# Optimization experiments

Hardware: AMD Instinct MI355X
Metric: run time of the kernel (lower is better)

## Reference

```python
import jax, jax.numpy as jnp
import numpy as np

B, G, K, KD = 16384, 17, 12, 16      # batch, games, kicks/game, kick feature dim
DK, DM, H, T = 16, 32, 2, 4          # d_kick, d_model, n_attn_heads, n_targets
SD, H1, H2, HH = 64, 256, 128, 32    # static_dim, backbone hidden dims, head hidden
AO = H * DM                          # attention output dim = 64
EPS = 1e-5
NEG_INF = float('-inf')


def setup_inputs() -> dict:
    ks = jax.random.split(jax.random.key(0), 18)
    n = lambda i, s, sc=0.05: jax.random.normal(ks[i], s, jnp.float32) * sc
    x_static = jax.random.normal(ks[0], (B, SD), jnp.float32)
    x_kicks = jax.random.normal(ks[1], (B, G, K, KD), jnp.float32)
    # masks: True = real game / kick; force position 0 valid so no row is fully padded
    outer_mask = jax.random.bernoulli(ks[2], 0.9, (B, G)).at[:, 0].set(True)
    inner_mask = jax.random.bernoulli(ks[3], 0.85, (B, G, K)).at[:, :, 0].set(True)
    return dict(
        x_static=x_static, x_kicks=x_kicks,
        W_ke=n(4, (KD, DK)), b_ke=jnp.zeros((DK,), jnp.float32),
        q_inner=n(5, (1, DK), 0.02),
        W_ge=n(6, (DK, DM)), b_ge=jnp.zeros((DM,), jnp.float32),
        pos_emb=n(7, (G, DM), 0.02),
        q_outer=n(8, (T * H, DM), 0.02),
        log_temp=jnp.zeros((T,), jnp.float32),
        ln_g=jnp.ones((T, AO), jnp.float32), ln_b=jnp.zeros((T, AO), jnp.float32),
        W1=n(9, (SD, H1)), b1=jnp.zeros((H1,), jnp.float32),
        g1=jnp.ones((H1,), jnp.float32), be1=jnp.zeros((H1,), jnp.float32),
        m1=n(10, (H1,)), v1=jax.random.uniform(ks[11], (H1,), jnp.float32) + 0.5,
        W2=n(12, (H1, H2)), b2=jnp.zeros((H2,), jnp.float32),
        g2=jnp.ones((H2,), jnp.float32), be2=jnp.zeros((H2,), jnp.float32),
        m2=n(13, (H2,)), v2=jax.random.uniform(ks[14], (H2,), jnp.float32) + 0.5,
        Wh1=n(15, (T, H2 + AO, HH)), bh1=jnp.zeros((T, HH), jnp.float32),
        Wh2=n(16, (T, HH)), bh2=jnp.zeros((T,), jnp.float32),
        outer_mask=outer_mask, inner_mask=inner_mask)


def _forward(x_static, x_kicks, W_ke, b_ke, q_inner, W_ge, b_ge, pos_emb,
             q_outer, log_temp, ln_g, ln_b, W1, b1, g1, be1, m1, v1,
             W2, b2, g2, be2, m2, v2, Wh1, bh1, Wh2, bh2,
             outer_mask, inner_mask):
    # kick encoder: Linear -> ReLU, [B,G,K,KD] -> [B,G,K,DK]
    kick_enc = jax.nn.relu(jnp.einsum('bgkd,de->bgke', x_kicks, W_ke) + b_ke)
    # inner AttentionPool: single learned query over kicks within each game
    ai = jnp.einsum('d,bgkd->bgk', q_inner[0], kick_enc) * (DK ** -0.5)
    ai = jnp.where(inner_mask, ai, NEG_INF)
    wi = jnp.nan_to_num(jax.nn.softmax(ai, axis=-1))       # all-masked rows -> 0
    per_game = jnp.einsum('bgk,bgkd->bgd', wi, kick_enc)   # [B,G,DK]
    # game encoder + learned positional embedding
    encoded = jax.nn.relu(per_game @ W_ge + b_ge) + pos_emb[None]  # [B,G,DM]
    # outer AttentionPool: T*H learned queries over games, per-target temperature
    ao = jnp.einsum('qd,bgd->bqg', q_outer, encoded) * (DM ** -0.5)
    ao = ao * jnp.repeat(jnp.exp(-log_temp), H)[None, :, None]
    ao = jnp.where(outer_mask[:, None, :], ao, NEG_INF)
    wo = jnp.nan_to_num(jax.nn.softmax(ao, axis=-1))
    pooled = jnp.einsum('bqg,bgd->bqd', wo, encoded).reshape(-1, T, AO)  # [B,T,64]
    # per-target LayerNorm on history vector
    mu = pooled.mean(-1, keepdims=True)
    var = ((pooled - mu) ** 2).mean(-1, keepdims=True)
    hist = (pooled - mu) * jax.lax.rsqrt(var + EPS) * ln_g[None] + ln_b[None]
    # backbone: Linear -> BatchNorm(eval) -> ReLU, x2 (dropout = identity in eval)
    z = jax.nn.relu((x_static @ W1 + b1 - m1) * jax.lax.rsqrt(v1 + EPS) * g1 + be1)
    z = jax.nn.relu((z @ W2 + b2 - m2) * jax.lax.rsqrt(v2 + EPS) * g2 + be2)
    # per-target heads on [shared_static ; history_vec]
    head_in = jnp.concatenate(
        [jnp.broadcast_to(z[:, None, :], (z.shape[0], T, H2)), hist], axis=-1)  # [B,T,192]
    h = jax.nn.relu(jnp.einsum('btd,tdh->bth', head_in, Wh1) + bh1[None])
    out = jnp.einsum('bth,th->bt', h, Wh2) + bh2[None]
    return jnp.maximum(out, 0.0)  # all targets non-negative (clamp, not softplus)


def reference(x_static, x_kicks, W_ke, b_ke, q_inner, W_ge, b_ge, pos_emb,
              q_outer, log_temp, ln_g, ln_b, W1, b1, g1, be1, m1, v1,
              W2, b2, g2, be2, m2, v2, Wh1, bh1, Wh2, bh2,
              outer_mask, inner_mask):
    return _forward(x_static, x_kicks, W_ke, b_ke, q_inner, W_ge, b_ge, pos_emb,
                    q_outer, log_temp, ln_g, ln_b, W1, b1, g1, be1, m1, v1,
                    W2, b2, g2, be2, m2, v2, Wh1, bh1, Wh2, bh2,
                    outer_mask, inner_mask)
```

## Files before the change

### kernel.cpp

```cpp
#include <hip/hip_runtime.h>
#include <math.h>

#define NEGM (-1e30f)

typedef __fp16 f16x4 __attribute__((ext_vector_type(4)));
typedef __fp16 f16x2 __attribute__((ext_vector_type(2)));
typedef float  f32x4 __attribute__((ext_vector_type(4)));

__device__ __forceinline__ float4 ld4(const float* p) { return *(const float4*)p; }
__device__ __forceinline__ void fma4(float4& a, float s, const float4 w) {
    a.x += s * w.x; a.y += s * w.y; a.z += s * w.z; a.w += s * w.w;
}

__global__ __launch_bounds__(64) void hist_kernel(
    const float* __restrict__ x_kicks,
    const float* __restrict__ W_ke, const float* __restrict__ b_ke,
    const float* __restrict__ q_inner,
    const float* __restrict__ W_ge, const float* __restrict__ b_ge,
    const float* __restrict__ pos_emb, const float* __restrict__ q_outer,
    const float* __restrict__ log_temp,
    const float* __restrict__ ln_g, const float* __restrict__ ln_b,
    const int* __restrict__ outer_mask, const int* __restrict__ inner_mask,
    float* __restrict__ hist)
{
    __shared__ float s_wge[512];
    __shared__ float s_qout[256];
    __shared__ float pg[17 * 20];
    __shared__ float enc[17 * 36];
    __shared__ float ao[136];
    __shared__ float s_S[20];

    const int lane = threadIdx.x;
    const int b    = blockIdx.x;
    const int jcol = lane & 15;
    const int g    = lane >> 4;
    const int kb   = g * 4;

    *(float4*)&s_wge[lane * 4]       = ld4(W_ge + lane * 4);
    *(float4*)&s_wge[256 + lane * 4] = ld4(W_ge + 256 + lane * 4);
    *(float4*)&s_qout[lane * 4]      = ld4(q_outer + lane * 4);

    f16x4 bw;
    #pragma unroll
    for (int jj = 0; jj < 4; ++jj)
        bw[jj] = (__fp16)W_ke[(kb + jj) * 16 + jcol];
    const float bias = b_ke[jcol];
    const f32x4 cinit = {bias, bias, bias, bias};
    const float qv = q_inner[jcol] * 0.25f;

    const float* xb = x_kicks + (size_t)b * 204 * 16;
    const int*   mb = inner_mask + (size_t)b * 204;

    f32x4 PG   = {0.f, 0.f, 0.f, 0.f};
    f32x4 PG16 = {0.f, 0.f, 0.f, 0.f};
    float Sacc = 0.f, S16 = 0.f;

    int g0 = (g == 3) ? 1 : 0;
    int p0 = (g == 3) ? 0 : 4 * g;

    #pragma unroll
    for (int t = 0; t < 12; ++t) {
        float4 xv = ld4(xb + (16 * t + jcol) * 16 + kb);
        int4 mv = *(const int4*)(mb + 16 * t + 4 * g);

        f16x2 xlo = __builtin_amdgcn_cvt_pkrtz(xv.x, xv.y);
        f16x2 xhi = __builtin_amdgcn_cvt_pkrtz(xv.z, xv.w);
        f16x4 ax; ax[0]=xlo[0]; ax[1]=xlo[1]; ax[2]=xhi[0]; ax[3]=xhi[1];

        f32x4 D1 = __builtin_amdgcn_mfma_f32_16x16x16f16(ax, bw, cinit, 0, 0, 0);
        #pragma unroll
        for (int jj = 0; jj < 4; ++jj) D1[jj] = fmaxf(D1[jj], 0.f);

        f16x2 pA = __builtin_amdgcn_cvt_pkrtz(D1[0] * qv, D1[1] * qv);
        f16x2 pB = __builtin_amdgcn_cvt_pkrtz(D1[2] * qv, D1[3] * qv);
        #pragma unroll
        for (int o = 1; o < 16; o <<= 1) {
            int ia = __shfl_xor(__builtin_bit_cast(int, pA), o);
            int ib = __shfl_xor(__builtin_bit_cast(int, pB), o);
            pA = pA + __builtin_bit_cast(f16x2, ia);
            pB = pB + __builtin_bit_cast(f16x2, ib);
        }
        float s0 = (float)pA[0], s1 = (float)pA[1];
        float s2 = (float)pB[0], s3 = (float)pB[1];

        f16x4 aw;
        #pragma unroll
        for (int jj = 0; jj < 4; ++jj) {
            int mk = (jj==0)?mv.x:(jj==1)?mv.y:(jj==2)?mv.z:mv.w;
            float sv = (jj==0)?s0:(jj==1)?s1:(jj==2)?s2:s3;
            float e = mk ? __expf(sv) : 0.f;
            int game_jj = g0 + ((p0 + jj) >= 12 ? 1 : 0);
            float w = (game_jj == jcol) ? e : 0.f;
            aw[jj] = (__fp16)w;
            Sacc += w;
        }
        g0 += 1; p0 += 4;
        if (p0 >= 12) { p0 -= 12; g0 += 1; }

        f16x2 elo = __builtin_amdgcn_cvt_pkrtz(D1[0], D1[1]);
        f16x2 ehi = __builtin_amdgcn_cvt_pkrtz(D1[2], D1[3]);
        f16x4 be; be[0]=elo[0]; be[1]=elo[1]; be[2]=ehi[0]; be[3]=ehi[1];

        PG = __builtin_amdgcn_mfma_f32_16x16x16f16(aw, be, PG, 0, 0, 0);
    }

    {
        int kidx = 192 + jcol;
        int kc = (kidx < 204) ? kidx : 203;
        float4 xv = ld4(xb + kc * 16 + kb);
        int km = 192 + 4 * g;
        int kmc = (km <= 200) ? km : 200;
        int4 mv = *(const int4*)(mb + kmc);

        f16x2 xlo = __builtin_amdgcn_cvt_pkrtz(xv.x, xv.y);
        f16x2 xhi = __builtin_amdgcn_cvt_pkrtz(xv.z, xv.w);
        f16x4 ax; ax[0]=xlo[0]; ax[1]=xlo[1]; ax[2]=xhi[0]; ax[3]=xhi[1];

        f32x4 D1 = __builtin_amdgcn_mfma_f32_16x16x16f16(ax, bw, cinit, 0, 0, 0);
        #pragma unroll
        for (int jj = 0; jj < 4; ++jj) D1[jj] = fmaxf(D1[jj], 0.f);

        f16x2 pA = __builtin_amdgcn_cvt_pkrtz(D1[0] * qv, D1[1] * qv);
        f16x2 pB = __builtin_amdgcn_cvt_pkrtz(D1[2] * qv, D1[3] * qv);
        #pragma unroll
        for (int o = 1; o < 16; o <<= 1) {
            int ia = __shfl_xor(__builtin_bit_cast(int, pA), o);
            int ib = __shfl_xor(__builtin_bit_cast(int, pB), o);
            pA = pA + __builtin_bit_cast(f16x2, ia);
            pB = pB + __builtin_bit_cast(f16x2, ib);
        }
        float s0 = (float)pA[0], s1 = (float)pA[1];
        float s2 = (float)pB[0], s3 = (float)pB[1];

        f16x4 aw2;
        #pragma unroll
        for (int jj = 0; jj < 4; ++jj) {
            int pos = 4 * g + jj;
            int mk = (jj==0)?mv.x:(jj==1)?mv.y:(jj==2)?mv.z:mv.w;
            float sv = (jj==0)?s0:(jj==1)?s1:(jj==2)?s2:s3;
            bool valid = (pos < 12) && mk;
            float e = valid ? __expf(sv) : 0.f;
            float w = (jcol == 0) ? e : 0.f;
            aw2[jj] = (__fp16)w;
            S16 += w;
        }

        f16x2 elo = __builtin_amdgcn_cvt_pkrtz(D1[0], D1[1]);
        f16x2 ehi = __builtin_amdgcn_cvt_pkrtz(D1[2], D1[3]);
        f16x4 be; be[0]=elo[0]; be[1]=elo[1]; be[2]=ehi[0]; be[3]=ehi[1];

        PG16 = __builtin_amdgcn_mfma_f32_16x16x16f16(aw2, be, PG16, 0, 0, 0);
    }

    Sacc += __shfl_xor(Sacc, 16);
    Sacc += __shfl_xor(Sacc, 32);
    S16 += __shfl_xor(S16, 16);
    S16 += __shfl_xor(S16, 32);

    if (lane < 16) s_S[lane] = Sacc;
    if (lane == 0) s_S[16] = S16;
    __syncthreads();

    #pragma unroll
    for (int jj = 0; jj < 4; ++jj) {
        int game = kb + jj;
        pg[game * 20 + jcol] = PG[jj] * (1.f / s_S[game]);
    }
    if (lane < 16) pg[16 * 20 + lane] = PG16[0] * (1.f / s_S[16]);
    __syncthreads();

    for (int t = lane; t < 136; t += 64) {
        const int gg = t >> 3, dq = t & 7;
        float4 acc = ld4(b_ge + dq * 4);
        #pragma unroll
        for (int i = 0; i < 16; ++i) {
            float pv = pg[gg * 20 + i];
            fma4(acc, pv, *(float4*)&s_wge[i * 32 + dq * 4]);
        }
        float4 pe = ld4(pos_emb + gg * 32 + dq * 4);
        acc.x = fmaxf(acc.x, 0.f) + pe.x; acc.y = fmaxf(acc.y, 0.f) + pe.y;
        acc.z = fmaxf(acc.z, 0.f) + pe.z; acc.w = fmaxf(acc.w, 0.f) + pe.w;
        *(float4*)&enc[gg * 36 + dq * 4] = acc;
    }
    __syncthreads();

    for (int t = lane; t < 136; t += 64) {
        const int q = t / 17, gg = t - q * 17;
        float4 acc = {0.f, 0.f, 0.f, 0.f};
        #pragma unroll
        for (int i4 = 0; i4 < 8; ++i4) {
            float4 ev = *(float4*)&enc[gg * 36 + i4 * 4];
            float4 qvv = *(float4*)&s_qout[q * 32 + i4 * 4];
            acc.x += ev.x * qvv.x; acc.y += ev.y * qvv.y;
            acc.z += ev.z * qvv.z; acc.w += ev.w * qvv.w;
        }
        float sv = (acc.x + acc.y) + (acc.z + acc.w);
        sv *= 0.17677669529663687f * __expf(-log_temp[q >> 1]);
        ao[t] = outer_mask[b * 17 + gg] ? sv : NEGM;
    }
    __syncthreads();

    {
        const int q = lane >> 3, j = lane & 7;
        float s0 = ao[q * 17 + j];
        float s1 = ao[q * 17 + j + 8];
        float s2 = (j == 0) ? ao[q * 17 + 16] : NEGM;
        float mx = fmaxf(fmaxf(s0, s1), s2);
        mx = fmaxf(mx, __shfl_xor(mx, 1));
        mx = fmaxf(mx, __shfl_xor(mx, 2));
        mx = fmaxf(mx, __shfl_xor(mx, 4));
        float e0 = __expf(s0 - mx), e1 = __expf(s1 - mx);
        float e2 = (j == 0) ? __expf(s2 - mx) : 0.f;
        float ssum = e0 + e1 + e2;
        ssum += __shfl_xor(ssum, 1);
        ssum += __shfl_xor(ssum, 2);
        ssum += __shfl_xor(ssum, 4);
        float inv = 1.f / ssum;
        ao[q * 17 + j] = e0 * inv;
        ao[q * 17 + j + 8] = e1 * inv;
        if (j == 0) ao[q * 17 + 16] = e2 * inv;
    }
    __syncthreads();

    {
        const int q = lane >> 3, dq = lane & 7;
        float4 acc = {0.f, 0.f, 0.f, 0.f};
        #pragma unroll
        for (int gg = 0; gg < 17; ++gg) {
            float w = ao[q * 17 + gg];
            fma4(acc, w, *(float4*)&enc[gg * 36 + dq * 4]);
        }
        float sv = (acc.x + acc.y) + (acc.z + acc.w);
        sv += __shfl_xor(sv, 1); sv += __shfl_xor(sv, 2);
        sv += __shfl_xor(sv, 4); sv += __shfl_xor(sv, 8);
        float mu = sv * 0.015625f;
        float4 d;
        d.x = acc.x - mu; d.y = acc.y - mu; d.z = acc.z - mu; d.w = acc.w - mu;
        float v = (d.x * d.x + d.y * d.y) + (d.z * d.z + d.w * d.w);
        v += __shfl_xor(v, 1); v += __shfl_xor(v, 2);
        v += __shfl_xor(v, 4); v += __shfl_xor(v, 8);
        float rs = rsqrtf(v * 0.015625f + 1e-5f);
        float4 gam = ld4(ln_g + lane * 4);
        float4 bet = ld4(ln_b + lane * 4);
        float4 res;
        res.x = d.x * rs * gam.x + bet.x; res.y = d.y * rs * gam.y + bet.y;
        res.z = d.z * rs * gam.z + bet.z; res.w = d.w * rs * gam.w + bet.w;
        *(float4*)&hist[(size_t)b * 256 + lane * 4] = res;
    }
}

__global__ __launch_bounds__(256) void backbone_kernel(
    const float* __restrict__ x_static,
    const float* __restrict__ W1, const float* __restrict__ b1,
    const float* __restrict__ g1, const float* __restrict__ be1,
    const float* __restrict__ m1, const float* __restrict__ v1,
    const float* __restrict__ W2, const float* __restrict__ b2,
    const float* __restrict__ g2, const float* __restrict__ be2,
    const float* __restrict__ m2, const float* __restrict__ v2,
    const float* __restrict__ Wh1, const float* __restrict__ bh1,
    const float* __restrict__ Wh2, const float* __restrict__ bh2,
    const float* __restrict__ hist, float* __restrict__ out)
{
    __shared__ float s_x[16 * 64];
    __shared__ float s_z1[16 * 256];
    __shared__ float s_z2[16 * 132];

    const int tid = threadIdx.x;
    const int row0 = blockIdx.x * 16;

    *(float4*)&s_x[tid * 4] = ld4(x_static + (size_t)row0 * 64 + tid * 4);
    __syncthreads();

    {
        const int col = tid;
        float acc[16];
        #pragma unroll
        for (int r = 0; r < 16; ++r) acc[r] = 0.f;
        for (int k4 = 0; k4 < 16; ++k4) {
            float w0 = W1[(k4 * 4 + 0) * 256 + col];
            float w1 = W1[(k4 * 4 + 1) * 256 + col];
            float w2 = W1[(k4 * 4 + 2) * 256 + col];
            float w3 = W1[(k4 * 4 + 3) * 256 + col];
            #pragma unroll
            for (int r = 0; r < 16; ++r) {
                float4 xv = *(float4*)&s_x[r * 64 + k4 * 4];
                acc[r] += xv.x * w0 + xv.y * w1 + xv.z * w2 + xv.w * w3;
            }
        }
        float sc = rsqrtf(v1[col] + 1e-5f) * g1[col];
        float off = b1[col] - m1[col];
        float bb = be1[col];
        #pragma unroll
        for (int r = 0; r < 16; ++r)
            s_z1[r * 256 + col] = fmaxf((acc[r] + off) * sc + bb, 0.f);
    }
    __syncthreads();

    {
        const int col = tid & 127;
        const int r0 = (tid >> 7) * 8;
        float acc[8];
        #pragma unroll
        for (int r = 0; r < 8; ++r) acc[r] = 0.f;
        for (int k4 = 0; k4 < 64; ++k4) {
            float w0 = W2[(k4 * 4 + 0) * 128 + col];
            float w1 = W2[(k4 * 4 + 1) * 128 + col];
            float w2 = W2[(k4 * 4 + 2) * 128 + col];
            float w3 = W2[(k4 * 4 + 3) * 128 + col];
            #pragma unroll
            for (int r = 0; r < 8; ++r) {
                float4 zv = *(float4*)&s_z1[(r0 + r) * 256 + k4 * 4];
                acc[r] += zv.x * w0 + zv.y * w1 + zv.z * w2 + zv.w * w3;
            }
        }
        float sc = rsqrtf(v2[col] + 1e-5f) * g2[col];
        float off = b2[col] - m2[col];
        float bb = be2[col];
        #pragma unroll
        for (int r = 0; r < 8; ++r)
            s_z2[(r0 + r) * 132 + col] = fmaxf((acc[r] + off) * sc + bb, 0.f);
    }
    __syncthreads();

    {
        const int p = tid >> 2;
        const int gl = tid & 3;
        const int row = p >> 2;
        const int tgt = p & 3;
        const int j0 = gl * 8;

        float acc[8];
        #pragma unroll
        for (int j = 0; j < 8; ++j) acc[j] = bh1[tgt * 32 + j0 + j];

        const float* w1p = Wh1 + (size_t)tgt * 192 * 32 + j0;
        for (int d4 = 0; d4 < 32; ++d4) {
            float4 zv = *(float4*)&s_z2[row * 132 + d4 * 4];
            #pragma unroll
            for (int c = 0; c < 4; ++c) {
                float v = (c == 0) ? zv.x : (c == 1) ? zv.y : (c == 2) ? zv.z : zv.w;
                float4 a = ld4(w1p + (d4 * 4 + c) * 32);
                float4 bq = ld4(w1p + (d4 * 4 + c) * 32 + 4);
                acc[0] += v * a.x;  acc[1] += v * a.y;  acc[2] += v * a.z;  acc[3] += v * a.w;
                acc[4] += v * bq.x; acc[5] += v * bq.y; acc[6] += v * bq.z; acc[7] += v * bq.w;
            }
        }
        const float* hp = hist + (size_t)(row0 + row) * 256 + tgt * 64;
        const float* w1q = w1p + 128 * 32;
        for (int d4 = 0; d4 < 16; ++d4) {
            float4 hv = ld4(hp + d4 * 4);
            #pragma unroll
            for (int c = 0; c < 4; ++c) {
                float v = (c == 0) ? hv.x : (c == 1) ? hv.y : (c == 2) ? hv.z : hv.w;
                float4 a = ld4(w1q + (d4 * 4 + c) * 32);
                float4 bq = ld4(w1q + (d4 * 4 + c) * 32 + 4);
                acc[0] += v * a.x;  acc[1] += v * a.y;  acc[2] += v * a.z;  acc[3] += v * a.w;
                acc[4] += v * bq.x; acc[5] += v * bq.y; acc[6] += v * bq.z; acc[7] += v * bq.w;
            }
        }
        float ps = 0.f;
        #pragma unroll
        for (int j = 0; j < 8; ++j) ps += fmaxf(acc[j], 0.f) * Wh2[tgt * 32 + j0 + j];
        ps += __shfl_xor(ps, 1);
        ps += __shfl_xor(ps, 2);
        if (gl == 0) out[(size_t)(row0 + row) * 4 + tgt] = fmaxf(ps + bh2[tgt], 0.f);
    }
}

extern "C" void kernel_launch(void* const* d_in, const int* in_sizes, int n_in,
                              void* d_out, int out_size, void* d_ws, size_t ws_size,
                              hipStream_t stream) {
    const float* x_static = (const float*)d_in[0];
    const float* x_kicks  = (const float*)d_in[1];
    const float* W_ke     = (const float*)d_in[2];
    const float* b_ke     = (const float*)d_in[3];
    const float* q_inner  = (const float*)d_in[4];
    const float* W_ge     = (const float*)d_in[5];
    const float* b_ge     = (const float*)d_in[6];
    const float* pos_emb  = (const float*)d_in[7];
    const float* q_outer  = (const float*)d_in[8];
    const float* log_temp = (const float*)d_in[9];
    const float* ln_g     = (const float*)d_in[10];
    const float* ln_b     = (const float*)d_in[11];
    const float* W1       = (const float*)d_in[12];
    const float* b1       = (const float*)d_in[13];
    const float* g1       = (const float*)d_in[14];
    const float* be1      = (const float*)d_in[15];
    const float* m1       = (const float*)d_in[16];
    const float* v1       = (const float*)d_in[17];
    const float* W2       = (const float*)d_in[18];
    const float* b2       = (const float*)d_in[19];
    const float* g2       = (const float*)d_in[20];
    const float* be2      = (const float*)d_in[21];
    const float* m2       = (const float*)d_in[22];
    const float* v2       = (const float*)d_in[23];
    const float* Wh1      = (const float*)d_in[24];
    const float* bh1      = (const float*)d_in[25];
    const float* Wh2      = (const float*)d_in[26];
    const float* bh2      = (const float*)d_in[27];
    const int* outer_mask = (const int*)d_in[28];
    const int* inner_mask = (const int*)d_in[29];

    float* hist = (float*)d_ws;
    float* out  = (float*)d_out;

    hist_kernel<<<16384, 64, 0, stream>>>(
        x_kicks, W_ke, b_ke, q_inner, W_ge, b_ge, pos_emb, q_outer,
        log_temp, ln_g, ln_b, outer_mask, inner_mask, hist);

    backbone_kernel<<<16384 / 16, 256, 0, stream>>>(
        x_static, W1, b1, g1, be1, m1, v1, W2, b2, g2, be2, m2, v2,
        Wh1, bh1, Wh2, bh2, hist, out);
}
```

Baseline: 138.6 us.

## Co-schedule history attention and static backbone in one heterogeneous kernel

Merges the per-sample history kernel and the static backbone MLP into one launch, interleaving block roles (4 history blocks per 1 backbone block). History blocks now hold 4 waves, one sample each, and share staged weights. The backbone output is written to a workspace buffer and a separate heads kernel consumes it with the history vectors. The aim is to overlap the memory-bound kick processing with the compute-bound backbone GEMMs. The cost is an extra global round trip for the backbone activations and a different occupancy profile from the larger shared-memory footprint.

```diff
diff --git a/kernel.cpp b/kernel.cpp
--- a/kernel.cpp
+++ b/kernel.cpp
@@ -12,7 +12,7 @@
     a.x += s * w.x; a.y += s * w.y; a.z += s * w.z; a.w += s * w.w;
 }
 
-__global__ __launch_bounds__(64) void hist_kernel(
+__global__ __launch_bounds__(256) void fused1_kernel(
     const float* __restrict__ x_kicks,
     const float* __restrict__ W_ke, const float* __restrict__ b_ke,
     const float* __restrict__ q_inner,
@@ -21,235 +21,6 @@
     const float* __restrict__ log_temp,
     const float* __restrict__ ln_g, const float* __restrict__ ln_b,
     const int* __restrict__ outer_mask, const int* __restrict__ inner_mask,
-    float* __restrict__ hist)
-{
-    __shared__ float s_wge[512];
-    __shared__ float s_qout[256];
-    __shared__ float pg[17 * 20];
-    __shared__ float enc[17 * 36];
-    __shared__ float ao[136];
-    __shared__ float s_S[20];
-
-    const int lane = threadIdx.x;
-    const int b    = blockIdx.x;
-    const int jcol = lane & 15;
-    const int g    = lane >> 4;
-    const int kb   = g * 4;
-
-    *(float4*)&s_wge[lane * 4]       = ld4(W_ge + lane * 4);
-    *(float4*)&s_wge[256 + lane * 4] = ld4(W_ge + 256 + lane * 4);
-    *(float4*)&s_qout[lane * 4]      = ld4(q_outer + lane * 4);
-
-    f16x4 bw;
-    #pragma unroll
-    for (int jj = 0; jj < 4; ++jj)
-        bw[jj] = (__fp16)W_ke[(kb + jj) * 16 + jcol];
-    const float bias = b_ke[jcol];
-    const f32x4 cinit = {bias, bias, bias, bias};
-    const float qv = q_inner[jcol] * 0.25f;
-
-    const float* xb = x_kicks + (size_t)b * 204 * 16;
-    const int*   mb = inner_mask + (size_t)b * 204;
-
-    f32x4 PG   = {0.f, 0.f, 0.f, 0.f};
-    f32x4 PG16 = {0.f, 0.f, 0.f, 0.f};
-    float Sacc = 0.f, S16 = 0.f;
-
-    int g0 = (g == 3) ? 1 : 0;
-    int p0 = (g == 3) ? 0 : 4 * g;
-
-    #pragma unroll
-    for (int t = 0; t < 12; ++t) {
-        float4 xv = ld4(xb + (16 * t + jcol) * 16 + kb);
-        int4 mv = *(const int4*)(mb + 16 * t + 4 * g);
-
-        f16x2 xlo = __builtin_amdgcn_cvt_pkrtz(xv.x, xv.y);
-        f16x2 xhi = __builtin_amdgcn_cvt_pkrtz(xv.z, xv.w);
-        f16x4 ax; ax[0]=xlo[0]; ax[1]=xlo[1]; ax[2]=xhi[0]; ax[3]=xhi[1];
-
-        f32x4 D1 = __builtin_amdgcn_mfma_f32_16x16x16f16(ax, bw, cinit, 0, 0, 0);
-        #pragma unroll
-        for (int jj = 0; jj < 4; ++jj) D1[jj] = fmaxf(D1[jj], 0.f);
-
-        f16x2 pA = __builtin_amdgcn_cvt_pkrtz(D1[0] * qv, D1[1] * qv);
-        f16x2 pB = __builtin_amdgcn_cvt_pkrtz(D1[2] * qv, D1[3] * qv);
-        #pragma unroll
-        for (int o = 1; o < 16; o <<= 1) {
-            int ia = __shfl_xor(__builtin_bit_cast(int, pA), o);
-            int ib = __shfl_xor(__builtin_bit_cast(int, pB), o);
-            pA = pA + __builtin_bit_cast(f16x2, ia);
-            pB = pB + __builtin_bit_cast(f16x2, ib);
-        }
-        float s0 = (float)pA[0], s1 = (float)pA[1];
-        float s2 = (float)pB[0], s3 = (float)pB[1];
-
-        f16x4 aw;
-        #pragma unroll
-        for (int jj = 0; jj < 4; ++jj) {
-            int mk = (jj==0)?mv.x:(jj==1)?mv.y:(jj==2)?mv.z:mv.w;
-            float sv = (jj==0)?s0:(jj==1)?s1:(jj==2)?s2:s3;
-            float e = mk ? __expf(sv) : 0.f;
-            int game_jj = g0 + ((p0 + jj) >= 12 ? 1 : 0);
-            float w = (game_jj == jcol) ? e : 0.f;
-            aw[jj] = (__fp16)w;
-            Sacc += w;
-        }
-        g0 += 1; p0 += 4;
-        if (p0 >= 12) { p0 -= 12; g0 += 1; }
-
-        f16x2 elo = __builtin_amdgcn_cvt_pkrtz(D1[0], D1[1]);
-        f16x2 ehi = __builtin_amdgcn_cvt_pkrtz(D1[2], D1[3]);
-        f16x4 be; be[0]=elo[0]; be[1]=elo[1]; be[2]=ehi[0]; be[3]=ehi[1];
-
-        PG = __builtin_amdgcn_mfma_f32_16x16x16f16(aw, be, PG, 0, 0, 0);
-    }
-
-    {
-        int kidx = 192 + jcol;
-        int kc = (kidx < 204) ? kidx : 203;
-        float4 xv = ld4(xb + kc * 16 + kb);
-        int km = 192 + 4 * g;
-        int kmc = (km <= 200) ? km : 200;
-        int4 mv = *(const int4*)(mb + kmc);
-
-        f16x2 xlo = __builtin_amdgcn_cvt_pkrtz(xv.x, xv.y);
-        f16x2 xhi = __builtin_amdgcn_cvt_pkrtz(xv.z, xv.w);
-        f16x4 ax; ax[0]=xlo[0]; ax[1]=xlo[1]; ax[2]=xhi[0]; ax[3]=xhi[1];
-
-        f32x4 D1 = __builtin_amdgcn_mfma_f32_16x16x16f16(ax, bw, cinit, 0, 0, 0);
-        #pragma unroll
-        for (int jj = 0; jj < 4; ++jj) D1[jj] = fmaxf(D1[jj], 0.f);
-
-        f16x2 pA = __builtin_amdgcn_cvt_pkrtz(D1[0] * qv, D1[1] * qv);
-        f16x2 pB = __builtin_amdgcn_cvt_pkrtz(D1[2] * qv, D1[3] * qv);
-        #pragma unroll
-        for (int o = 1; o < 16; o <<= 1) {
-            int ia = __shfl_xor(__builtin_bit_cast(int, pA), o);
-            int ib = __shfl_xor(__builtin_bit_cast(int, pB), o);
-            pA = pA + __builtin_bit_cast(f16x2, ia);
-            pB = pB + __builtin_bit_cast(f16x2, ib);
-        }
-        float s0 = (float)pA[0], s1 = (float)pA[1];
-        float s2 = (float)pB[0], s3 = (float)pB[1];
-
-        f16x4 aw2;
-        #pragma unroll
-        for (int jj = 0; jj < 4; ++jj) {
-            int pos = 4 * g + jj;
-            int mk = (jj==0)?mv.x:(jj==1)?mv.y:(jj==2)?mv.z:mv.w;
-            float sv = (jj==0)?s0:(jj==1)?s1:(jj==2)?s2:s3;
-            bool valid = (pos < 12) && mk;
-            float e = valid ? __expf(sv) : 0.f;
-            float w = (jcol == 0) ? e : 0.f;
-            aw2[jj] = (__fp16)w;
-            S16 += w;
-        }
-
-        f16x2 elo = __builtin_amdgcn_cvt_pkrtz(D1[0], D1[1]);
-        f16x2 ehi = __builtin_amdgcn_cvt_pkrtz(D1[2], D1[3]);
-        f16x4 be; be[0]=elo[0]; be[1]=elo[1]; be[2]=ehi[0]; be[3]=ehi[1];
-
-        PG16 = __builtin_amdgcn_mfma_f32_16x16x16f16(aw2, be, PG16, 0, 0, 0);
-    }
-
-    Sacc += __shfl_xor(Sacc, 16);
-    Sacc += __shfl_xor(Sacc, 32);
-    S16 += __shfl_xor(S16, 16);
-    S16 += __shfl_xor(S16, 32);
-
-    if (lane < 16) s_S[lane] = Sacc;
-    if (lane == 0) s_S[16] = S16;
-    __syncthreads();
-
-    #pragma unroll
-    for (int jj = 0; jj < 4; ++jj) {
-        int game = kb + jj;
-        pg[game * 20 + jcol] = PG[jj] * (1.f / s_S[game]);
-    }
-    if (lane < 16) pg[16 * 20 + lane] = PG16[0] * (1.f / s_S[16]);
-    __syncthreads();
-
-    for (int t = lane; t < 136; t += 64) {
-        const int gg = t >> 3, dq = t & 7;
-        float4 acc = ld4(b_ge + dq * 4);
-        #pragma unroll
-        for (int i = 0; i < 16; ++i) {
-            float pv = pg[gg * 20 + i];
-            fma4(acc, pv, *(float4*)&s_wge[i * 32 + dq * 4]);
-        }
-        float4 pe = ld4(pos_emb + gg * 32 + dq * 4);
-        acc.x = fmaxf(acc.x, 0.f) + pe.x; acc.y = fmaxf(acc.y, 0.f) + pe.y;
-        acc.z = fmaxf(acc.z, 0.f) + pe.z; acc.w = fmaxf(acc.w, 0.f) + pe.w;
-        *(float4*)&enc[gg * 36 + dq * 4] = acc;
-    }
-    __syncthreads();
-
-    for (int t = lane; t < 136; t += 64) {
-        const int q = t / 17, gg = t - q * 17;
-        float4 acc = {0.f, 0.f, 0.f, 0.f};
-        #pragma unroll
-        for (int i4 = 0; i4 < 8; ++i4) {
-            float4 ev = *(float4*)&enc[gg * 36 + i4 * 4];
-            float4 qvv = *(float4*)&s_qout[q * 32 + i4 * 4];
-            acc.x += ev.x * qvv.x; acc.y += ev.y * qvv.y;
-            acc.z += ev.z * qvv.z; acc.w += ev.w * qvv.w;
-        }
-        float sv = (acc.x + acc.y) + (acc.z + acc.w);
-        sv *= 0.17677669529663687f * __expf(-log_temp[q >> 1]);
-        ao[t] = outer_mask[b * 17 + gg] ? sv : NEGM;
-    }
-    __syncthreads();
-
-    {
-        const int q = lane >> 3, j = lane & 7;
-        float s0 = ao[q * 17 + j];
-        float s1 = ao[q * 17 + j + 8];
-        float s2 = (j == 0) ? ao[q * 17 + 16] : NEGM;
-        float mx = fmaxf(fmaxf(s0, s1), s2);
-        mx = fmaxf(mx, __shfl_xor(mx, 1));
-        mx = fmaxf(mx, __shfl_xor(mx, 2));
-        mx = fmaxf(mx, __shfl_xor(mx, 4));
-        float e0 = __expf(s0 - mx), e1 = __expf(s1 - mx);
-        float e2 = (j == 0) ? __expf(s2 - mx) : 0.f;
-        float ssum = e0 + e1 + e2;
-        ssum += __shfl_xor(ssum, 1);
-        ssum += __shfl_xor(ssum, 2);
-        ssum += __shfl_xor(ssum, 4);
-        float inv = 1.f / ssum;
-        ao[q * 17 + j] = e0 * inv;
-        ao[q * 17 + j + 8] = e1 * inv;
-        if (j == 0) ao[q * 17 + 16] = e2 * inv;
-    }
-    __syncthreads();
-
-    {
-        const int q = lane >> 3, dq = lane & 7;
-        float4 acc = {0.f, 0.f, 0.f, 0.f};
-        #pragma unroll
-        for (int gg = 0; gg < 17; ++gg) {
-            float w = ao[q * 17 + gg];
-            fma4(acc, w, *(float4*)&enc[gg * 36 + dq * 4]);
-        }
-        float sv = (acc.x + acc.y) + (acc.z + acc.w);
-        sv += __shfl_xor(sv, 1); sv += __shfl_xor(sv, 2);
-        sv += __shfl_xor(sv, 4); sv += __shfl_xor(sv, 8);
-        float mu = sv * 0.015625f;
-        float4 d;
-        d.x = acc.x - mu; d.y = acc.y - mu; d.z = acc.z - mu; d.w = acc.w - mu;
-        float v = (d.x * d.x + d.y * d.y) + (d.z * d.z + d.w * d.w);
-        v += __shfl_xor(v, 1); v += __shfl_xor(v, 2);
-        v += __shfl_xor(v, 4); v += __shfl_xor(v, 8);
-        float rs = rsqrtf(v * 0.015625f + 1e-5f);
-        float4 gam = ld4(ln_g + lane * 4);
-        float4 bet = ld4(ln_b + lane * 4);
-        float4 res;
-        res.x = d.x * rs * gam.x + bet.x; res.y = d.y * rs * gam.y + bet.y;
-        res.z = d.z * rs * gam.z + bet.z; res.w = d.w * rs * gam.w + bet.w;
-        *(float4*)&hist[(size_t)b * 256 + lane * 4] = res;
-    }
-}
-
-__global__ __launch_bounds__(256) void backbone_kernel(
     const float* __restrict__ x_static,
     const float* __restrict__ W1, const float* __restrict__ b1,
     const float* __restrict__ g1, const float* __restrict__ be1,
@@ -257,114 +28,363 @@
     const float* __restrict__ W2, const float* __restrict__ b2,
     const float* __restrict__ g2, const float* __restrict__ be2,
     const float* __restrict__ m2, const float* __restrict__ v2,
+    float* __restrict__ hist, float* __restrict__ zbuf)
+{
+    __shared__ float smem[5200];
+    const int tid = threadIdx.x;
+    const int q5 = blockIdx.x / 5;
+    const int r5 = blockIdx.x - q5 * 5;
+
+    if (r5 < 4) {
+        const int hb   = q5 * 4 + r5;
+        const int wid  = tid >> 6;
+        const int lane = tid & 63;
+        const int b    = hb * 4 + wid;
+        const int jcol = lane & 15;
+        const int g    = lane >> 4;
+        const int kb   = g * 4;
+
+        float* s_wge  = smem;
+        float* s_qout = smem + 512;
+        float* scr = smem + 768 + wid * 1108;
+        float* pg  = scr;
+        float* enc = scr + 340;
+        float* ao  = scr + 952;
+        float* sS  = scr + 1088;
+
+        s_wge[tid] = W_ge[tid];
+        s_wge[tid + 256] = W_ge[tid + 256];
+        s_qout[tid] = q_outer[tid];
+        __syncthreads();
+
+        f16x4 bw;
+        #pragma unroll
+        for (int jj = 0; jj < 4; ++jj)
+            bw[jj] = (__fp16)W_ke[(kb + jj) * 16 + jcol];
+        const float bias = b_ke[jcol];
+        const f32x4 cinit = {bias, bias, bias, bias};
+        const float qv = q_inner[jcol] * 0.25f;
+
+        const float* xb = x_kicks + (size_t)b * 204 * 16;
+        const int*   mb = inner_mask + (size_t)b * 204;
+
+        f32x4 PG   = {0.f, 0.f, 0.f, 0.f};
+        f32x4 PG16 = {0.f, 0.f, 0.f, 0.f};
+        float Sacc = 0.f, S16 = 0.f;
+
+        int g0 = (g == 3) ? 1 : 0;
+        int p0 = (g == 3) ? 0 : 4 * g;
+
+        #pragma unroll
+        for (int t = 0; t < 12; ++t) {
+            float4 xv = ld4(xb + (16 * t + jcol) * 16 + kb);
+            int4 mv = *(const int4*)(mb + 16 * t + 4 * g);
+
+            f16x2 xlo = __builtin_amdgcn_cvt_pkrtz(xv.x, xv.y);
+            f16x2 xhi = __builtin_amdgcn_cvt_pkrtz(xv.z, xv.w);
+            f16x4 ax; ax[0]=xlo[0]; ax[1]=xlo[1]; ax[2]=xhi[0]; ax[3]=xhi[1];
+
+            f32x4 D1 = __builtin_amdgcn_mfma_f32_16x16x16f16(ax, bw, cinit, 0, 0, 0);
+            #pragma unroll
+            for (int jj = 0; jj < 4; ++jj) D1[jj] = fmaxf(D1[jj], 0.f);
+
+            f16x2 pA = __builtin_amdgcn_cvt_pkrtz(D1[0] * qv, D1[1] * qv);
+            f16x2 pB = __builtin_amdgcn_cvt_pkrtz(D1[2] * qv, D1[3] * qv);
+            #pragma unroll
+            for (int o = 1; o < 16; o <<= 1) {
+                int ia = __shfl_xor(__builtin_bit_cast(int, pA), o);
+                int ib = __shfl_xor(__builtin_bit_cast(int, pB), o);
+                pA = pA + __builtin_bit_cast(f16x2, ia);
+                pB = pB + __builtin_bit_cast(f16x2, ib);
+            }
+            float s0 = (float)pA[0], s1 = (float)pA[1];
+            float s2 = (float)pB[0], s3 = (float)pB[1];
+
+            f16x4 aw;
+            #pragma unroll
+            for (int jj = 0; jj < 4; ++jj) {
+                int mk = (jj==0)?mv.x:(jj==1)?mv.y:(jj==2)?mv.z:mv.w;
+                float sv = (jj==0)?s0:(jj==1)?s1:(jj==2)?s2:s3;
+                float e = mk ? __expf(sv) : 0.f;
+                int game_jj = g0 + ((p0 + jj) >= 12 ? 1 : 0);
+                float w = (game_jj == jcol) ? e : 0.f;
+                aw[jj] = (__fp16)w;
+                Sacc += w;
+            }
+            g0 += 1; p0 += 4;
+            if (p0 >= 12) { p0 -= 12; g0 += 1; }
+
+            f16x2 elo = __builtin_amdgcn_cvt_pkrtz(D1[0], D1[1]);
+            f16x2 ehi = __builtin_amdgcn_cvt_pkrtz(D1[2], D1[3]);
+            f16x4 be; be[0]=elo[0]; be[1]=elo[1]; be[2]=ehi[0]; be[3]=ehi[1];
+
+            PG = __builtin_amdgcn_mfma_f32_16x16x16f16(aw, be, PG, 0, 0, 0);
+        }
+
+        {
+            int kidx = 192 + jcol;
+            int kc = (kidx < 204) ? kidx : 203;
+            float4 xv = ld4(xb + kc * 16 + kb);
+            int km = 192 + 4 * g;
+            int kmc = (km <= 200) ? km : 200;
+            int4 mv = *(const int4*)(mb + kmc);
+
+            f16x2 xlo = __builtin_amdgcn_cvt_pkrtz(xv.x, xv.y);
+            f16x2 xhi = __builtin_amdgcn_cvt_pkrtz(xv.z, xv.w);
+            f16x4 ax; ax[0]=xlo[0]; ax[1]=xlo[1]; ax[2]=xhi[0]; ax[3]=xhi[1];
+
+            f32x4 D1 = __builtin_amdgcn_mfma_f32_16x16x16f16(ax, bw, cinit, 0, 0, 0);
+            #pragma unroll
+            for (int jj = 0; jj < 4; ++jj) D1[jj] = fmaxf(D1[jj], 0.f);
+
+            f16x2 pA = __builtin_amdgcn_cvt_pkrtz(D1[0] * qv, D1[1] * qv);
+            f16x2 pB = __builtin_amdgcn_cvt_pkrtz(D1[2] * qv, D1[3] * qv);
+            #pragma unroll
+            for (int o = 1; o < 16; o <<= 1) {
+                int ia = __shfl_xor(__builtin_bit_cast(int, pA), o);
+                int ib = __shfl_xor(__builtin_bit_cast(int, pB), o);
+                pA = pA + __builtin_bit_cast(f16x2, ia);
+                pB = pB + __builtin_bit_cast(f16x2, ib);
+            }
+            float s0 = (float)pA[0], s1 = (float)pA[1];
+            float s2 = (float)pB[0], s3 = (float)pB[1];
+
+            f16x4 aw2;
+            #pragma unroll
+            for (int jj = 0; jj < 4; ++jj) {
+                int pos = 4 * g + jj;
+                int mk = (jj==0)?mv.x:(jj==1)?mv.y:(jj==2)?mv.z:mv.w;
+                float sv = (jj==0)?s0:(jj==1)?s1:(jj==2)?s2:s3;
+                bool valid = (pos < 12) && mk;
+                float e = valid ? __expf(sv) : 0.f;
+                float w = (jcol == 0) ? e : 0.f;
+                aw2[jj] = (__fp16)w;
+                S16 += w;
+            }
+
+            f16x2 elo = __builtin_amdgcn_cvt_pkrtz(D1[0], D1[1]);
+            f16x2 ehi = __builtin_amdgcn_cvt_pkrtz(D1[2], D1[3]);
+            f16x4 be; be[0]=elo[0]; be[1]=elo[1]; be[2]=ehi[0]; be[3]=ehi[1];
+
+            PG16 = __builtin_amdgcn_mfma_f32_16x16x16f16(aw2, be, PG16, 0, 0, 0);
+        }
+
+        Sacc += __shfl_xor(Sacc, 16);
+        Sacc += __shfl_xor(Sacc, 32);
+        S16 += __shfl_xor(S16, 16);
+        S16 += __shfl_xor(S16, 32);
+
+        if (lane < 16) sS[lane] = Sacc;
+        if (lane == 0) sS[16] = S16;
+        __syncthreads();
+
+        #pragma unroll
+        for (int jj = 0; jj < 4; ++jj) {
+            int game = kb + jj;
+            pg[game * 20 + jcol] = PG[jj] * (1.f / sS[game]);
+        }
+        if (lane < 16) pg[16 * 20 + lane] = PG16[0] * (1.f / sS[16]);
+        __syncthreads();
+
+        for (int t = lane; t < 136; t += 64) {
+            const int gg = t >> 3, dq = t & 7;
+            float4 acc = ld4(b_ge + dq * 4);
+            #pragma unroll
+            for (int i = 0; i < 16; ++i) {
+                float pv = pg[gg * 20 + i];
+                fma4(acc, pv, *(float4*)&s_wge[i * 32 + dq * 4]);
+            }
+            float4 pe = ld4(pos_emb + gg * 32 + dq * 4);
+            acc.x = fmaxf(acc.x, 0.f) + pe.x; acc.y = fmaxf(acc.y, 0.f) + pe.y;
+            acc.z = fmaxf(acc.z, 0.f) + pe.z; acc.w = fmaxf(acc.w, 0.f) + pe.w;
+            *(float4*)&enc[gg * 36 + dq * 4] = acc;
+        }
+        __syncthreads();
+
+        for (int t = lane; t < 136; t += 64) {
+            const int q = t / 17, gg = t - q * 17;
+            float4 acc = {0.f, 0.f, 0.f, 0.f};
+            #pragma unroll
+            for (int i4 = 0; i4 < 8; ++i4) {
+                float4 ev = *(float4*)&enc[gg * 36 + i4 * 4];
+                float4 qvv = *(float4*)&s_qout[q * 32 + i4 * 4];
+                acc.x += ev.x * qvv.x; acc.y += ev.y * qvv.y;
+                acc.z += ev.z * qvv.z; acc.w += ev.w * qvv.w;
+            }
+            float sv = (acc.x + acc.y) + (acc.z + acc.w);
+            sv *= 0.17677669529663687f * __expf(-log_temp[q >> 1]);
+            ao[t] = outer_mask[b * 17 + gg] ? sv : NEGM;
+        }
+        __syncthreads();
+
+        {
+            const int q = lane >> 3, j = lane & 7;
+            float s0 = ao[q * 17 + j];
+            float s1 = ao[q * 17 + j + 8];
+            float s2 = (j == 0) ? ao[q * 17 + 16] : NEGM;
+            float mx = fmaxf(fmaxf(s0, s1), s2);
+            mx = fmaxf(mx, __shfl_xor(mx, 1));
+            mx = fmaxf(mx, __shfl_xor(mx, 2));
+            mx = fmaxf(mx, __shfl_xor(mx, 4));
+            float e0 = __expf(s0 - mx), e1 = __expf(s1 - mx);
+            float e2 = (j == 0) ? __expf(s2 - mx) : 0.f;
+            float ssum = e0 + e1 + e2;
+            ssum += __shfl_xor(ssum, 1);
+            ssum += __shfl_xor(ssum, 2);
+            ssum += __shfl_xor(ssum, 4);
+            float inv = 1.f / ssum;
+            ao[q * 17 + j] = e0 * inv;
+            ao[q * 17 + j + 8] = e1 * inv;
+            if (j == 0) ao[q * 17 + 16] = e2 * inv;
+        }
+        __syncthreads();
+
+        {
+            const int q = lane >> 3, dq = lane & 7;
+            float4 acc = {0.f, 0.f, 0.f, 0.f};
+            #pragma unroll
+            for (int gg = 0; gg < 17; ++gg) {
+                float w = ao[q * 17 + gg];
+                fma4(acc, w, *(float4*)&enc[gg * 36 + dq * 4]);
+            }
+            float sv = (acc.x + acc.y) + (acc.z + acc.w);
+            sv += __shfl_xor(sv, 1); sv += __shfl_xor(sv, 2);
+            sv += __shfl_xor(sv, 4); sv += __shfl_xor(sv, 8);
+            float mu = sv * 0.015625f;
+            float4 d;
+            d.x = acc.x - mu; d.y = acc.y - mu; d.z = acc.z - mu; d.w = acc.w - mu;
+            float v = (d.x * d.x + d.y * d.y) + (d.z * d.z + d.w * d.w);
+            v += __shfl_xor(v, 1); v += __shfl_xor(v, 2);
+            v += __shfl_xor(v, 4); v += __shfl_xor(v, 8);
+            float rs = rsqrtf(v * 0.015625f + 1e-5f);
+            float4 gam = ld4(ln_g + lane * 4);
+            float4 bet = ld4(ln_b + lane * 4);
+            float4 res;
+            res.x = d.x * rs * gam.x + bet.x; res.y = d.y * rs * gam.y + bet.y;
+            res.z = d.z * rs * gam.z + bet.z; res.w = d.w * rs * gam.w + bet.w;
+            *(float4*)&hist[(size_t)b * 256 + lane * 4] = res;
+        }
+    } else {
+        const int row0 = q5 * 16;
+        float* s_x  = smem;
+        float* s_z1 = smem + 1024;
+
+        *(float4*)&s_x[tid * 4] = ld4(x_static + (size_t)row0 * 64 + tid * 4);
+        __syncthreads();
+
+        {
+            const int col = tid;
+            float acc[16];
+            #pragma unroll
+            for (int r = 0; r < 16; ++r) acc[r] = 0.f;
+            for (int k4 = 0; k4 < 16; ++k4) {
+                float w0 = W1[(k4 * 4 + 0) * 256 + col];
+                float w1 = W1[(k4 * 4 + 1) * 256 + col];
+                float w2 = W1[(k4 * 4 + 2) * 256 + col];
+                float w3 = W1[(k4 * 4 + 3) * 256 + col];
+                #pragma unroll
+                for (int r = 0; r < 16; ++r) {
+                    float4 xv = *(float4*)&s_x[r * 64 + k4 * 4];
+                    acc[r] += xv.x * w0 + xv.y * w1 + xv.z * w2 + xv.w * w3;
+                }
+            }
+            float sc = rsqrtf(v1[col] + 1e-5f) * g1[col];
+            float off = b1[col] - m1[col];
+            float bb = be1[col];
+            #pragma unroll
+            for (int r = 0; r < 16; ++r)
+                s_z1[r * 256 + col] = fmaxf((acc[r] + off) * sc + bb, 0.f);
+        }
+        __syncthreads();
+
+        {
+            const int col = tid & 127;
+            const int r0 = (tid >> 7) * 8;
+            float acc[8];
+            #pragma unroll
+            for (int r = 0; r < 8; ++r) acc[r] = 0.f;
+            for (int k4 = 0; k4 < 64; ++k4) {
+                float w0 = W2[(k4 * 4 + 0) * 128 + col];
+                float w1 = W2[(k4 * 4 + 1) * 128 + col];
+                float w2 = W2[(k4 * 4 + 2) * 128 + col];
+                float w3 = W2[(k4 * 4 + 3) * 128 + col];
+                #pragma unroll
+                for (int r = 0; r < 8; ++r) {
+                    float4 zv = *(float4*)&s_z1[(r0 + r) * 256 + k4 * 4];
+                    acc[r] += zv.x * w0 + zv.y * w1 + zv.z * w2 + zv.w * w3;
+                }
+            }
+            float sc = rsqrtf(v2[col] + 1e-5f) * g2[col];
+            float off = b2[col] - m2[col];
+            float bb = be2[col];
+            #pragma unroll
+            for (int r = 0; r < 8; ++r)
+                zbuf[(size_t)(row0 + r0 + r) * 128 + col] =
+                    fmaxf((acc[r] + off) * sc + bb, 0.f);
+        }
+    }
+}
+
+__global__ __launch_bounds__(256) void heads_kernel(
+    const float* __restrict__ zbuf, const float* __restrict__ hist,
     const float* __restrict__ Wh1, const float* __restrict__ bh1,
     const float* __restrict__ Wh2, const float* __restrict__ bh2,
-    const float* __restrict__ hist, float* __restrict__ out)
+    float* __restrict__ out)
 {
-    __shared__ float s_x[16 * 64];
-    __shared__ float s_z1[16 * 256];
     __shared__ float s_z2[16 * 132];
-
     const int tid = threadIdx.x;
     const int row0 = blockIdx.x * 16;
 
-    *(float4*)&s_x[tid * 4] = ld4(x_static + (size_t)row0 * 64 + tid * 4);
-    __syncthreads();
-
     {
-        const int col = tid;
-        float acc[16];
-        #pragma unroll
-        for (int r = 0; r < 16; ++r) acc[r] = 0.f;
-        for (int k4 = 0; k4 < 16; ++k4) {
-            float w0 = W1[(k4 * 4 + 0) * 256 + col];
-            float w1 = W1[(k4 * 4 + 1) * 256 + col];
-            float w2 = W1[(k4 * 4 + 2) * 256 + col];
-            float w3 = W1[(k4 * 4 + 3) * 256 + col];
-            #pragma unroll
-            for (int r = 0; r < 16; ++r) {
-                float4 xv = *(float4*)&s_x[r * 64 + k4 * 4];
-                acc[r] += xv.x * w0 + xv.y * w1 + xv.z * w2 + xv.w * w3;
-            }
-        }
-        float sc = rsqrtf(v1[col] + 1e-5f) * g1[col];
-        float off = b1[col] - m1[col];
-        float bb = be1[col];
-        #pragma unroll
-        for (int r = 0; r < 16; ++r)
-            s_z1[r * 256 + col] = fmaxf((acc[r] + off) * sc + bb, 0.f);
+        const int r = tid >> 4, c = (tid & 15) * 8;
+        float4 v0 = ld4(zbuf + (size_t)(row0 + r) * 128 + c);
+        float4 v1 = ld4(zbuf + (size_t)(row0 + r) * 128 + c + 4);
+        *(float4*)&s_z2[r * 132 + c] = v0;
+        *(float4*)&s_z2[r * 132 + c + 4] = v1;
     }
     __syncthreads();
 
-    {
-        const int col = tid & 127;
-        const int r0 = (tid >> 7) * 8;
-        float acc[8];
+    const int p = tid >> 2;
+    const int gl = tid & 3;
+    const int row = p >> 2;
+    const int tgt = p & 3;
+    const int j0 = gl * 8;
+
+    float acc[8];
+    #pragma unroll
+    for (int j = 0; j < 8; ++j) acc[j] = bh1[tgt * 32 + j0 + j];
+
+    const float* w1p = Wh1 + (size_t)tgt * 192 * 32 + j0;
+    for (int d4 = 0; d4 < 32; ++d4) {
+        float4 zv = *(float4*)&s_z2[row * 132 + d4 * 4];
         #pragma unroll
-        for (int r = 0; r < 8; ++r) acc[r] = 0.f;
-        for (int k4 = 0; k4 < 64; ++k4) {
-            float w0 = W2[(k4 * 4 + 0) * 128 + col];
-            float w1 = W2[(k4 * 4 + 1) * 128 + col];
-            float w2 = W2[(k4 * 4 + 2) * 128 + col];
-            float w3 = W2[(k4 * 4 + 3) * 128 + col];
-            #pragma unroll
-            for (int r = 0; r < 8; ++r) {
-                float4 zv = *(float4*)&s_z1[(r0 + r) * 256 + k4 * 4];
-                acc[r] += zv.x * w0 + zv.y * w1 + zv.z * w2 + zv.w * w3;
-            }
-        }
-        float sc = rsqrtf(v2[col] + 1e-5f) * g2[col];
-        float off = b2[col] - m2[col];
-        float bb = be2[col];
+        for (int c = 0; c < 4; ++c) {
+            float v = (c == 0) ? zv.x : (c == 1) ? zv.y : (c == 2) ? zv.z : zv.w;
+            float4 a = ld4(w1p + (d4 * 4 + c) * 32);
+            float4 bq = ld4(w1p + (d4 * 4 + c) * 32 + 4);
+            acc[0] += v * a.x;  acc[1] += v * a.y;  acc[2] += v * a.z;  acc[3] += v * a.w;
+            acc[4] += v * bq.x; acc[5] += v * bq.y; acc[6] += v * bq.z; acc[7] += v * bq.w;
+        }
+    }
+    const float* hp = hist + (size_t)(row0 + row) * 256 + tgt * 64;
+    const float* w1q = w1p + 128 * 32;
+    for (int d4 = 0; d4 < 16; ++d4) {
+        float4 hv = ld4(hp + d4 * 4);
         #pragma unroll
-        for (int r = 0; r < 8; ++r)
-            s_z2[(r0 + r) * 132 + col] = fmaxf((acc[r] + off) * sc + bb, 0.f);
+        for (int c = 0; c < 4; ++c) {
+            float v = (c == 0) ? hv.x : (c == 1) ? hv.y : (c == 2) ? hv.z : hv.w;
+            float4 a = ld4(w1q + (d4 * 4 + c) * 32);
+            float4 bq = ld4(w1q + (d4 * 4 + c) * 32 + 4);
+            acc[0] += v * a.x;  acc[1] += v * a.y;  acc[2] += v * a.z;  acc[3] += v * a.w;
+            acc[4] += v * bq.x; acc[5] += v * bq.y; acc[6] += v * bq.z; acc[7] += v * bq.w;
+        }
     }
-    __syncthreads();
-
-    {
-        const int p = tid >> 2;
-        const int gl = tid & 3;
-        const int row = p >> 2;
-        const int tgt = p & 3;
-        const int j0 = gl * 8;
-
-        float acc[8];
-        #pragma unroll
-        for (int j = 0; j < 8; ++j) acc[j] = bh1[tgt * 32 + j0 + j];
-
-        const float* w1p = Wh1 + (size_t)tgt * 192 * 32 + j0;
-        for (int d4 = 0; d4 < 32; ++d4) {
-            float4 zv = *(float4*)&s_z2[row * 132 + d4 * 4];
-            #pragma unroll
-            for (int c = 0; c < 4; ++c) {
-                float v = (c == 0) ? zv.x : (c == 1) ? zv.y : (c == 2) ? zv.z : zv.w;
-                float4 a = ld4(w1p + (d4 * 4 + c) * 32);
-                float4 bq = ld4(w1p + (d4 * 4 + c) * 32 + 4);
-                acc[0] += v * a.x;  acc[1] += v * a.y;  acc[2] += v * a.z;  acc[3] += v * a.w;
-                acc[4] += v * bq.x; acc[5] += v * bq.y; acc[6] += v * bq.z; acc[7] += v * bq.w;
-            }
-        }
-        const float* hp = hist + (size_t)(row0 + row) * 256 + tgt * 64;
-        const float* w1q = w1p + 128 * 32;
-        for (int d4 = 0; d4 < 16; ++d4) {
-            float4 hv = ld4(hp + d4 * 4);
-            #pragma unroll
-            for (int c = 0; c < 4; ++c) {
-                float v = (c == 0) ? hv.x : (c == 1) ? hv.y : (c == 2) ? hv.z : hv.w;
-                float4 a = ld4(w1q + (d4 * 4 + c) * 32);
-                float4 bq = ld4(w1q + (d4 * 4 + c) * 32 + 4);
-                acc[0] += v * a.x;  acc[1] += v * a.y;  acc[2] += v * a.z;  acc[3] += v * a.w;
-                acc[4] += v * bq.x; acc[5] += v * bq.y; acc[6] += v * bq.z; acc[7] += v * bq.w;
-            }
-        }
-        float ps = 0.f;
-        #pragma unroll
-        for (int j = 0; j < 8; ++j) ps += fmaxf(acc[j], 0.f) * Wh2[tgt * 32 + j0 + j];
-        ps += __shfl_xor(ps, 1);
-        ps += __shfl_xor(ps, 2);
-        if (gl == 0) out[(size_t)(row0 + row) * 4 + tgt] = fmaxf(ps + bh2[tgt], 0.f);
-    }
+    float ps = 0.f;
+    #pragma unroll
+    for (int j = 0; j < 8; ++j) ps += fmaxf(acc[j], 0.f) * Wh2[tgt * 32 + j0 + j];
+    ps += __shfl_xor(ps, 1);
+    ps += __shfl_xor(ps, 2);
+    if (gl == 0) out[(size_t)(row0 + row) * 4 + tgt] = fmaxf(ps + bh2[tgt], 0.f);
 }
 
 extern "C" void kernel_launch(void* const* d_in, const int* in_sizes, int n_in,
@@ -402,13 +422,15 @@
     const int* inner_mask = (const int*)d_in[29];
 
     float* hist = (float*)d_ws;
+    float* zbuf = hist + (size_t)16384 * 256;
     float* out  = (float*)d_out;
 
-    hist_kernel<<<16384, 64, 0, stream>>>(
+    fused1_kernel<<<5120, 256, 0, stream>>>(
         x_kicks, W_ke, b_ke, q_inner, W_ge, b_ge, pos_emb, q_outer,
-        log_temp, ln_g, ln_b, outer_mask, inner_mask, hist);
-
-    backbone_kernel<<<16384 / 16, 256, 0, stream>>>(
+        log_temp, ln_g, ln_b, outer_mask, inner_mask,
         x_static, W1, b1, g1, be1, m1, v1, W2, b2, g2, be2, m2, v2,
-        Wh1, bh1, Wh2, bh2, hist, out);
+        hist, zbuf);
+
+    heads_kernel<<<1024, 256, 0, stream>>>(
+        zbuf, hist, Wh1, bh1, Wh2, bh2, out);
 }
```

Result: slower. 156.5 us (+12.9%).
